# Kernel optimization log

Hardware: AMD Instinct MI355X
Metric: run time of the kernel (lower is better)

Reference implementation:

```python
import jax, jax.numpy as jnp
import numpy as np

HID = 4096
HEADS = 32
HEAD_DIM = 128
SEQ = 2048
GROUP = 128          # AWQ quantization group size along the input (K) dim
QKV_OUT = 3 * HID
ROPE_BASE = 10000.0


def dequant(qweight, scales, zeros):
    # qweight: [K, N] int; scales/zeros: [K//GROUP, N]
    s = jnp.repeat(scales, GROUP, axis=0)
    z = jnp.repeat(zeros, GROUP, axis=0)
    return (qweight.astype(jnp.float32) - z) * s


def rotate_half(x):
    x1, x2 = jnp.split(x, 2, axis=-1)
    return jnp.concatenate((-x2, x1), axis=-1)


def setup_inputs() -> dict:
    key = jax.random.key(0)
    ks = jax.random.split(key, 8)
    hidden_states = jax.random.normal(ks[0], (1, SEQ, HID), dtype=jnp.float32)
    position_ids = jnp.arange(SEQ, dtype=jnp.int32)[None, :]
    qkv_qweight = jax.random.randint(ks[1], (HID, QKV_OUT), 0, 16, dtype=jnp.int32)
    qkv_scales = jax.random.uniform(ks[2], (HID // GROUP, QKV_OUT), dtype=jnp.float32) * 0.002
    qkv_zeros = jax.random.uniform(ks[3], (HID // GROUP, QKV_OUT), dtype=jnp.float32) * 16.0
    o_qweight = jax.random.randint(ks[4], (HID, HID), 0, 16, dtype=jnp.int32)
    o_scales = jax.random.uniform(ks[5], (HID // GROUP, HID), dtype=jnp.float32) * 0.002
    o_zeros = jax.random.uniform(ks[6], (HID // GROUP, HID), dtype=jnp.float32) * 16.0
    return {"hidden_states": hidden_states, "position_ids": position_ids,
            "qkv_qweight": qkv_qweight, "qkv_scales": qkv_scales, "qkv_zeros": qkv_zeros,
            "o_qweight": o_qweight, "o_scales": o_scales, "o_zeros": o_zeros}


def reference(hidden_states, position_ids, qkv_qweight, qkv_scales, qkv_zeros,
              o_qweight, o_scales, o_zeros):
    b, s, _ = hidden_states.shape
    # --- quantized QKV projection (dequant + GEMM) ---
    w_qkv = dequant(qkv_qweight, qkv_scales, qkv_zeros)        # [HID, 3*HID]
    proj = jnp.einsum('bsk,kn->bsn', hidden_states, w_qkv)     # [b, s, 3*HID]
    xqkv = proj.reshape(b, s, 3, HEADS, HEAD_DIM)
    # [b, h, s, d]
    q = jnp.transpose(xqkv[:, :, 0], (0, 2, 1, 3))
    k = jnp.transpose(xqkv[:, :, 1], (0, 2, 1, 3))
    v = jnp.transpose(xqkv[:, :, 2], (0, 2, 1, 3))
    # --- rotary embedding (no KV cache: kv_seq_len == s) ---
    inv_freq = 1.0 / (ROPE_BASE ** (jnp.arange(0, HEAD_DIM, 2, dtype=jnp.float32) / HEAD_DIM))
    t = jnp.arange(s, dtype=jnp.float32)
    freqs = jnp.outer(t, inv_freq)                             # [s, d/2]
    emb = jnp.concatenate((freqs, freqs), axis=-1)             # [s, d]
    cos = jnp.cos(emb)[position_ids][:, None]                  # [b, 1, s, d]
    sin = jnp.sin(emb)[position_ids][:, None]
    q = q * cos + rotate_half(q) * sin
    k = k * cos + rotate_half(k) * sin
    # --- causal attention (flash_attn_func, padding_mask=None branch) ---
    scale = 1.0 / jnp.sqrt(jnp.float32(HEAD_DIM))
    scores = jnp.einsum('bhqd,bhkd->bhqk', q, k) * scale       # [b, h, s, s]
    causal = jnp.tril(jnp.ones((s, s), dtype=bool))
    scores = jnp.where(causal, scores, jnp.float32(-1e30))
    probs = jax.nn.softmax(scores, axis=-1)
    attn = jnp.einsum('bhqk,bhkd->bhqd', probs, v)             # [b, h, s, d]
    attn = jnp.transpose(attn, (0, 2, 1, 3)).reshape(b, s, HID)
    # --- quantized output projection ---
    w_o = dequant(o_qweight, o_scales, o_zeros)                # [HID, HID]
    out = jnp.einsum('bsk,kn->bsn', attn, w_o)                 # [b, s, HID]
    return out
```

## Files before the change

### kernel.cpp

```cpp
#include <hip/hip_runtime.h>
#include <hip/hip_bf16.h>

#define S_LEN 2048
#define HID_DIM 4096
#define NH 32
#define HD 128
#define NQKV 12288

typedef _Float16 half2v __attribute__((ext_vector_type(2)));
typedef _Float16 half4v __attribute__((ext_vector_type(4)));
typedef _Float16 half8v __attribute__((ext_vector_type(8)));
typedef float f32x4 __attribute__((ext_vector_type(4)));

typedef const __attribute__((address_space(1))) unsigned int* gas_u32;
typedef __attribute__((address_space(3))) unsigned int* las_u32;

__device__ inline void g2lds16(const _Float16* g, _Float16* l) {
  __builtin_amdgcn_global_load_lds((gas_u32)g, (las_u32)l, 16, 0, 0);
}

__global__ __launch_bounds__(256) void dequant_w(const int* __restrict__ W,
                                                 const float* __restrict__ scal,
                                                 const float* __restrict__ zer,
                                                 _Float16* __restrict__ Wt, int K, int N) {
  __shared__ _Float16 lT[64 * 84];
  const int k0 = blockIdx.y * 64, n0 = blockIdx.x * 64;
  const int tid = threadIdx.x, c = tid & 63, rp = tid >> 6;
  const int g = k0 >> 7;
  const float sc = scal[(size_t)g * N + n0 + c];
  const float zp = zer[(size_t)g * N + n0 + c];
#pragma unroll
  for (int i = 0; i < 8; ++i) {
    const int k = i * 8 + rp * 2;
    const float q0 = (float)W[(size_t)(k0 + k) * N + n0 + c];
    const float q1 = (float)W[(size_t)(k0 + k + 1) * N + n0 + c];
    half2v p;
    p[0] = (_Float16)((q0 - zp) * sc);
    p[1] = (_Float16)((q1 - zp) * sc);
    *(half2v*)&lT[c * 84 + k] = p;
  }
  __syncthreads();
  const int kc = tid & 7, nr0 = tid >> 3;
#pragma unroll
  for (int i = 0; i < 2; ++i) {
    const int n = nr0 + 32 * i;
    union { half8v v8; half4v v4[2]; } u;
    u.v4[0] = *(const half4v*)&lT[n * 84 + kc * 8];
    u.v4[1] = *(const half4v*)&lT[n * 84 + kc * 8 + 4];
    *(half8v*)&Wt[(size_t)(n0 + n) * K + k0 + kc * 8] = u.v8;
  }
}

__global__ __launch_bounds__(256) void conv_a(const float* __restrict__ A, _Float16* __restrict__ Af) {
  const int i = blockIdx.x * 256 + threadIdx.x;
  const float4 t = ((const float4*)A)[i];
  half4v r;
  r[0] = (_Float16)t.x; r[1] = (_Float16)t.y; r[2] = (_Float16)t.z; r[3] = (_Float16)t.w;
  ((half4v*)Af)[i] = r;
}

__device__ inline void stage128x64(const _Float16* __restrict__ gp, int K,
                                   _Float16* lp, int wave, int stR, int stC) {
  g2lds16(gp + (size_t)(wave * 16 + stR) * K + stC, lp + (wave * 2) * 512);
  g2lds16(gp + (size_t)(wave * 16 + 8 + stR) * K + stC, lp + (wave * 2 + 1) * 512);
}

template <typename CT>
__global__ __launch_bounds__(512, 2) void gemm_f16(const _Float16* __restrict__ A,
                                                   const _Float16* __restrict__ Bt,
                                                   CT* __restrict__ C, int M, int N, int K) {
  __shared__ _Float16 sA[3][2][128 * 64];
  __shared__ _Float16 sB[2][128 * 64];

  const int tid = threadIdx.x;
  const int wave = tid >> 6, lane = tid & 63;
  const int quad = lane >> 4, l16 = lane & 15;
  const int wr = wave >> 2;
  const int wc = wave & 3;
  const int NT = K >> 6;

  const _Float16* Ab = A + (size_t)(blockIdx.y * 256) * K;
  const _Float16* Bb = Bt + (size_t)(blockIdx.x * 128) * K;

  const int stR = lane >> 3;
  const int stC = ((lane & 7) ^ stR) << 3;
  const int fx = l16 & 7;

#define LDA8(buf, half, r, c) (*(const half8v*)&sA[buf][half][(r) * 64 + (((c) ^ fx) << 3)])
#define LDB8(buf, r, c) (*(const half8v*)&sB[buf][(r) * 64 + (((c) ^ fx) << 3)])

  f32x4 acc[8][2];
  const f32x4 zero4 = {0.f, 0.f, 0.f, 0.f};
#pragma unroll
  for (int am = 0; am < 8; ++am)
#pragma unroll
    for (int nb = 0; nb < 2; ++nb) acc[am][nb] = zero4;

  stage128x64(Ab, K, &sA[0][0][0], wave, stR, stC);
  stage128x64(Ab + (size_t)128 * K, K, &sA[0][1][0], wave, stR, stC);
  stage128x64(Bb, K, &sB[0][0], wave, stR, stC);
  stage128x64(Ab + 64, K, &sA[1][0][0], wave, stR, stC);
  stage128x64(Ab + (size_t)128 * K + 64, K, &sA[1][1][0], wave, stR, stC);
  stage128x64(Bb + 64, K, &sB[1][0], wave, stR, stC);
  asm volatile("s_waitcnt vmcnt(6)" ::: "memory");
  __builtin_amdgcn_s_barrier();

  int bA = 0;
  for (int t = 0; t < NT; ++t) {
    const int bB = t & 1;
    const int bA2 = (bA + 2 >= 3) ? bA - 1 : bA + 2;

    half8v af[4][2], bf[2][2];
#pragma unroll
    for (int mb = 0; mb < 4; ++mb)
#pragma unroll
      for (int ks = 0; ks < 2; ++ks)
        af[mb][ks] = LDA8(bA, wr, mb * 16 + l16, ks * 4 + quad);
#pragma unroll
    for (int nb = 0; nb < 2; ++nb)
#pragma unroll
      for (int ks = 0; ks < 2; ++ks)
        bf[nb][ks] = LDB8(bB, wc * 32 + nb * 16 + l16, ks * 4 + quad);
    if (t + 2 < NT) {
      const _Float16* Ap = Ab + (size_t)(t + 2) * 64;
      stage128x64(Ap, K, &sA[bA2][0][0], wave, stR, stC);
      stage128x64(Ap + (size_t)128 * K, K, &sA[bA2][1][0], wave, stR, stC);
    }
    __builtin_amdgcn_s_barrier();
    asm volatile("s_waitcnt lgkmcnt(0)" ::: "memory");
    __builtin_amdgcn_sched_barrier(0);
    __builtin_amdgcn_s_setprio(1);
#pragma unroll
    for (int mb = 0; mb < 4; ++mb)
#pragma unroll
      for (int nb = 0; nb < 2; ++nb)
#pragma unroll
        for (int ks = 0; ks < 2; ++ks)
          acc[mb][nb] =
              __builtin_amdgcn_mfma_f32_16x16x32_f16(af[mb][ks], bf[nb][ks], acc[mb][nb], 0, 0, 0);
    __builtin_amdgcn_s_setprio(0);
    __builtin_amdgcn_s_barrier();

#pragma unroll
    for (int mb = 0; mb < 4; ++mb)
#pragma unroll
      for (int ks = 0; ks < 2; ++ks)
        af[mb][ks] = LDA8(bA, wr, 64 + mb * 16 + l16, ks * 4 + quad);
    if (t + 2 < NT) {
      stage128x64(Bb + (size_t)(t + 2) * 64, K, &sB[bB][0], wave, stR, stC);
      asm volatile("s_waitcnt vmcnt(6)" ::: "memory");
    } else if (t + 1 < NT) {
      asm volatile("s_waitcnt vmcnt(0)" ::: "memory");
    }
    __builtin_amdgcn_s_barrier();
    asm volatile("s_waitcnt lgkmcnt(0)" ::: "memory");
    __builtin_amdgcn_sched_barrier(0);
    __builtin_amdgcn_s_setprio(1);
#pragma unroll
    for (int mb = 0; mb < 4; ++mb)
#pragma unroll
      for (int nb = 0; nb < 2; ++nb)
#pragma unroll
        for (int ks = 0; ks < 2; ++ks)
          acc[4 + mb][nb] = __builtin_amdgcn_mfma_f32_16x16x32_f16(af[mb][ks], bf[nb][ks],
                                                                   acc[4 + mb][nb], 0, 0, 0);
    __builtin_amdgcn_s_setprio(0);
    __builtin_amdgcn_s_barrier();

    bA = (bA + 1 >= 3) ? 0 : bA + 1;
  }

  const int rbase = blockIdx.y * 256 + wr * 128 + quad * 4;
  const int cbase = blockIdx.x * 128 + wc * 32 + l16;
#pragma unroll
  for (int am = 0; am < 8; ++am)
#pragma unroll
    for (int nb = 0; nb < 2; ++nb)
#pragma unroll
      for (int i = 0; i < 4; ++i)
        C[(size_t)(rbase + am * 16 + i) * N + cbase + nb * 16] = (CT)acc[am][nb][i];
#undef LDA8
#undef LDB8
}

__global__ __launch_bounds__(256) void rope_kernel(const _Float16* __restrict__ proj,
                                                   const int* __restrict__ pos,
                                                   _Float16* __restrict__ Q, _Float16* __restrict__ K,
                                                   _Float16* __restrict__ Vt) {
  const int h = blockIdx.x, sb = blockIdx.y;
  const int tid = threadIdx.x;
  const int s0 = sb * 64;

#pragma unroll
  for (int it = 0; it < 16; ++it) {
    const int idx = it * 256 + tid;
    const int sl = idx >> 6, j = idx & 63;
    const int s = s0 + sl;
    const float p = (float)pos[s];
    const float invrev = exp2f(-0.20762050593045455f * (float)j) * 0.15915494309189535f;
    const float rev = p * invrev;
    const float frac = rev - floorf(rev);
    const float sn = __builtin_amdgcn_sinf(frac);
    const float cs = __builtin_amdgcn_cosf(frac);
    const _Float16* rp = proj + (size_t)s * NQKV + h * HD;
    {
      const float x1 = (float)rp[j], x2 = (float)rp[j + 64];
      _Float16* qp = Q + ((size_t)h * S_LEN + s) * HD;
      qp[j] = (_Float16)(x1 * cs - x2 * sn);
      qp[j + 64] = (_Float16)(x2 * cs + x1 * sn);
    }
    {
      const float x1 = (float)rp[HID_DIM + j], x2 = (float)rp[HID_DIM + j + 64];
      _Float16* kp = K + ((size_t)h * S_LEN + s) * HD;
      kp[j] = (_Float16)(x1 * cs - x2 * sn);
      kp[j + 64] = (_Float16)(x2 * cs + x1 * sn);
    }
  }

  __shared__ _Float16 lV[64 * 132];
#pragma unroll
  for (int r = 0; r < 4; ++r) {
    const int cid = r * 256 + tid;
    const int sl = cid >> 4;
    const int d0 = (cid & 15) * 8;
    const _Float16* vp = proj + (size_t)(s0 + sl) * NQKV + 2 * HID_DIM + h * HD + d0;
    *(half4v*)&lV[sl * 132 + d0] = *(const half4v*)vp;
    *(half4v*)&lV[sl * 132 + d0 + 4] = *(const half4v*)(vp + 4);
  }
  __syncthreads();
#pragma unroll
  for (int it = 0; it < 32; ++it) {
    const int d = it * 4 + (tid >> 6);
    const int sl = tid & 63;
    Vt[((size_t)h * HD + d) * S_LEN + s0 + sl] = lV[sl * 132 + d];
  }
}

__global__ __launch_bounds__(256) void flash_attn(const _Float16* __restrict__ Q,
                                                  const _Float16* __restrict__ Km,
                                                  const _Float16* __restrict__ Vt,
                                                  _Float16* __restrict__ O) {
  __shared__ _Float16 lK[32 * 128];
  __shared__ _Float16 lV[128 * 32];
  __shared__ _Float16 lP[4][2][16 * 40];
  const int h = blockIdx.y;
  const int xb = blockIdx.x;
  const int qb = (xb & 1) ? (15 - (xb >> 1)) : (xb >> 1);
  const int tid = threadIdx.x;
  const int wave = tid >> 6, lane = tid & 63;
  const int quad = lane >> 4, l16 = lane & 15;
  const int q0w = qb * 128 + wave * 32;
  const float scale = 0.08838834764831845f;

  const _Float16* Qh = Q + (size_t)h * S_LEN * HD;
  const _Float16* Kh = Km + (size_t)h * S_LEN * HD;
  const _Float16* Vh = Vt + (size_t)h * HD * S_LEN;

  const int kRow0 = wave * 8 + (lane >> 4);
  const int kSlot = lane & 15;
  const int vRow0 = wave * 32 + (lane >> 2);
  const int vSlot = lane & 3;

  half8v qf[2][4];
#pragma unroll
  for (int r = 0; r < 2; ++r)
#pragma unroll
    for (int c = 0; c < 4; ++c)
      qf[r][c] = *(const half8v*)&Qh[(size_t)(q0w + r * 16 + l16) * HD + c * 32 + quad * 8];

  const f32x4 zero4 = {0.f, 0.f, 0.f, 0.f};
  f32x4 o[2][8];
  f32x4 lp[2];
#pragma unroll
  for (int r = 0; r < 2; ++r) {
    lp[r] = zero4;
#pragma unroll
    for (int c = 0; c < 8; ++c) o[r][c] = zero4;
  }

  const int ntiles = 4 * qb + 4;
  for (int kt = 0; kt < ntiles; ++kt) {
#pragma unroll
    for (int i = 0; i < 2; ++i) {
      const int row = kRow0 + i * 4;
      const int ck = kSlot ^ (row & 15);
      g2lds16(Kh + (size_t)(kt * 32 + row) * HD + ck * 8, &lK[(wave * 8 + i * 4) * 128]);
    }
#pragma unroll
    for (int i = 0; i < 2; ++i) {
      const int row = vRow0 + i * 16;
      const int cv = vSlot ^ ((row >> 1) & 3);
      g2lds16(Vh + (size_t)row * S_LEN + kt * 32 + cv * 8, &lV[(wave * 32 + i * 16) * 32]);
    }
    __syncthreads();

    half8v kf[2][4];
#pragma unroll
    for (int hf = 0; hf < 2; ++hf)
#pragma unroll
      for (int c = 0; c < 4; ++c) {
        const int slot = (c * 4 + quad) ^ l16;
        kf[hf][c] = *(const half8v*)&lK[(hf * 16 + l16) * 128 + slot * 8];
      }
    half8v vf[8];
#pragma unroll
    for (int c = 0; c < 8; ++c) {
      const int slot = quad ^ ((l16 >> 1) & 3);
      vf[c] = *(const half8v*)&lV[(c * 16 + l16) * 32 + slot * 8];
    }

    f32x4 s[2][2];
#pragma unroll
    for (int r = 0; r < 2; ++r)
#pragma unroll
      for (int hf = 0; hf < 2; ++hf) {
        s[r][hf] = zero4;
#pragma unroll
        for (int c = 0; c < 4; ++c)
          s[r][hf] = __builtin_amdgcn_mfma_f32_16x16x32_f16(qf[r][c], kf[hf][c], s[r][hf], 0, 0, 0);
      }

#pragma unroll
    for (int r = 0; r < 2; ++r) {
      float p0[4], p1[4];
#pragma unroll
      for (int i = 0; i < 4; ++i) {
        const int row = q0w + r * 16 + quad * 4 + i;
        const int col0 = kt * 32 + l16, col1 = col0 + 16;
        const float e0 = __expf(s[r][0][i] * scale);
        const float e1 = __expf(s[r][1][i] * scale);
        p0[i] = (col0 <= row) ? e0 : 0.f;
        p1[i] = (col1 <= row) ? e1 : 0.f;
        lp[r][i] += p0[i] + p1[i];
      }
      _Float16* pw = lP[wave][r];
#pragma unroll
      for (int i = 0; i < 4; ++i) {
        pw[(quad * 4 + i) * 40 + l16] = (_Float16)p0[i];
        pw[(quad * 4 + i) * 40 + l16 + 16] = (_Float16)p1[i];
      }
    }
    half8v pa[2];
#pragma unroll
    for (int r = 0; r < 2; ++r) pa[r] = *(half8v*)&lP[wave][r][l16 * 40 + quad * 8];

#pragma unroll
    for (int c = 0; c < 8; ++c)
#pragma unroll
      for (int r = 0; r < 2; ++r)
        o[r][c] = __builtin_amdgcn_mfma_f32_16x16x32_f16(pa[r], vf[c], o[r][c], 0, 0, 0);

    __syncthreads();
  }

#pragma unroll
  for (int r = 0; r < 2; ++r) {
    f32x4 ls = lp[r];
#pragma unroll
    for (int off = 1; off < 16; off <<= 1) {
#pragma unroll
      for (int i = 0; i < 4; ++i) ls[i] += __shfl_xor(ls[i], off);
    }
    f32x4 inv;
#pragma unroll
    for (int i = 0; i < 4; ++i) inv[i] = 1.f / ls[i];
#pragma unroll
    for (int c = 0; c < 8; ++c) {
#pragma unroll
      for (int i = 0; i < 4; ++i) {
        const int row = q0w + r * 16 + quad * 4 + i;
        O[(size_t)row * HID_DIM + h * HD + c * 16 + l16] = (_Float16)(o[r][c][i] * inv[i]);
      }
    }
  }
}

extern "C" void kernel_launch(void* const* d_in, const int* in_sizes, int n_in,
                              void* d_out, int out_size, void* d_ws, size_t ws_size,
                              hipStream_t stream) {
  const float* hidden = (const float*)d_in[0];
  const int* pos = (const int*)d_in[1];
  const int* qkv_w = (const int*)d_in[2];
  const float* qkv_s = (const float*)d_in[3];
  const float* qkv_z = (const float*)d_in[4];
  const int* o_w = (const int*)d_in[5];
  const float* o_s = (const float*)d_in[6];
  const float* o_z = (const float*)d_in[7];

  char* ws = (char*)d_ws;
  _Float16* Wt_qkv = (_Float16*)(ws + 0);
  _Float16* Qb = (_Float16*)(ws + 0);
  _Float16* Kb = (_Float16*)(ws + 16777216);
  _Float16* Vtb = (_Float16*)(ws + 33554432);
  _Float16* Af16 = (_Float16*)(ws + 100663296);
  _Float16* attn = (_Float16*)(ws + 100663296);
  _Float16* proj = (_Float16*)(ws + 117440512);
  _Float16* Wt_o = (_Float16*)(ws + 117440512);
  float* out = (float*)d_out;

  hipLaunchKernelGGL(dequant_w, dim3(192, 64), dim3(256), 0, stream,
                     qkv_w, qkv_s, qkv_z, Wt_qkv, 4096, 12288);
  hipLaunchKernelGGL(conv_a, dim3(8192), dim3(256), 0, stream, hidden, Af16);
  hipLaunchKernelGGL((gemm_f16<_Float16>), dim3(96, 8), dim3(512), 0, stream,
                     Af16, Wt_qkv, proj, 2048, 12288, 4096);
  hipLaunchKernelGGL(rope_kernel, dim3(32, 32), dim3(256), 0, stream, proj, pos, Qb, Kb, Vtb);
  hipLaunchKernelGGL(dequant_w, dim3(64, 64), dim3(256), 0, stream,
                     o_w, o_s, o_z, Wt_o, 4096, 4096);
  hipLaunchKernelGGL(flash_attn, dim3(16, 32), dim3(256), 0, stream, Qb, Kb, Vtb, attn);
  hipLaunchKernelGGL((gemm_f16<float>), dim3(32, 8), dim3(512), 0, stream,
                     attn, Wt_o, out, 2048, 4096, 4096);
}
```

Baseline: 770.1 us.

## Widen QKV GEMM N-tile, restructure GEMM B prefetch, pipeline flash-attn KV loads

The GEMM is templated on the N-tile width. The QKV projection now uses a 256x192 tile, giving 512 blocks in place of 768, and B is prefetched one k-step ahead in 64-row chunks with one fewer barrier per phase. Flash attention gains a 4-deep LDS ring for K/V tiles staged two iterations ahead, with vmcnt waits replacing the per-tile __syncthreads pair, so global loads overlap compute. The costs are more accumulator registers in the GEMM, more LDS in attention (which can lower occupancy), and a tail wave-quantization effect for the QKV grid.

```diff
diff --git a/kernel.cpp b/kernel.cpp
--- a/kernel.cpp
+++ b/kernel.cpp
@@ -64,13 +64,17 @@
   g2lds16(gp + (size_t)(wave * 16 + stR) * K + stC, lp + (wave * 2) * 512);
   g2lds16(gp + (size_t)(wave * 16 + 8 + stR) * K + stC, lp + (wave * 2 + 1) * 512);
 }
-
-template <typename CT>
-__global__ __launch_bounds__(512, 2) void gemm_f16(const _Float16* __restrict__ A,
+__device__ inline void stage64x64(const _Float16* __restrict__ gp, int K,
+                                  _Float16* lp, int wave, int stR, int stC) {
+  g2lds16(gp + (size_t)(wave * 8 + stR) * K + stC, lp + wave * 512);
+}
+
+template <int NBF, typename CT>
+__global__ __launch_bounds__(512, 2) void gemm_2ph(const _Float16* __restrict__ A,
                                                    const _Float16* __restrict__ Bt,
                                                    CT* __restrict__ C, int M, int N, int K) {
   __shared__ _Float16 sA[3][2][128 * 64];
-  __shared__ _Float16 sB[2][128 * 64];
+  __shared__ _Float16 sB[2][NBF * 64 * 64];
 
   const int tid = threadIdx.x;
   const int wave = tid >> 6, lane = tid & 63;
@@ -80,107 +84,110 @@
   const int NT = K >> 6;
 
   const _Float16* Ab = A + (size_t)(blockIdx.y * 256) * K;
-  const _Float16* Bb = Bt + (size_t)(blockIdx.x * 128) * K;
+  const _Float16* Bb = Bt + (size_t)(blockIdx.x * (NBF * 64)) * K;
 
   const int stR = lane >> 3;
   const int stC = ((lane & 7) ^ stR) << 3;
   const int fx = l16 & 7;
 
-#define LDA8(buf, half, r, c) (*(const half8v*)&sA[buf][half][(r) * 64 + (((c) ^ fx) << 3)])
-#define LDB8(buf, r, c) (*(const half8v*)&sB[buf][(r) * 64 + (((c) ^ fx) << 3)])
-
-  f32x4 acc[8][2];
+#define COFF(ks_) ((((ks_) * 4 + quad) ^ fx) << 3)
+#define SYNC_MFMA()                                  \
+  __builtin_amdgcn_s_barrier();                      \
+  asm volatile("s_waitcnt lgkmcnt(0)" ::: "memory"); \
+  __builtin_amdgcn_sched_barrier(0);
+
+  f32x4 acc[8][NBF];
   const f32x4 zero4 = {0.f, 0.f, 0.f, 0.f};
 #pragma unroll
-  for (int am = 0; am < 8; ++am)
-#pragma unroll
-    for (int nb = 0; nb < 2; ++nb) acc[am][nb] = zero4;
-
+  for (int m8 = 0; m8 < 8; ++m8)
+#pragma unroll
+    for (int nb = 0; nb < NBF; ++nb) acc[m8][nb] = zero4;
+
+#pragma unroll
+  for (int j = 0; j < NBF; ++j)
+    stage64x64(Bb + (size_t)(j * 64) * K, K, &sB[0][j * 4096], wave, stR, stC);
   stage128x64(Ab, K, &sA[0][0][0], wave, stR, stC);
   stage128x64(Ab + (size_t)128 * K, K, &sA[0][1][0], wave, stR, stC);
-  stage128x64(Bb, K, &sB[0][0], wave, stR, stC);
   stage128x64(Ab + 64, K, &sA[1][0][0], wave, stR, stC);
   stage128x64(Ab + (size_t)128 * K + 64, K, &sA[1][1][0], wave, stR, stC);
-  stage128x64(Bb + 64, K, &sB[1][0], wave, stR, stC);
-  asm volatile("s_waitcnt vmcnt(6)" ::: "memory");
+  asm volatile("s_waitcnt vmcnt(4)" ::: "memory");
   __builtin_amdgcn_s_barrier();
 
   int bA = 0;
   for (int t = 0; t < NT; ++t) {
     const int bB = t & 1;
     const int bA2 = (bA + 2 >= 3) ? bA - 1 : bA + 2;
-
-    half8v af[4][2], bf[2][2];
+    half8v af[4][2], bf[NBF][2];
+
 #pragma unroll
     for (int mb = 0; mb < 4; ++mb)
 #pragma unroll
       for (int ks = 0; ks < 2; ++ks)
-        af[mb][ks] = LDA8(bA, wr, mb * 16 + l16, ks * 4 + quad);
-#pragma unroll
-    for (int nb = 0; nb < 2; ++nb)
+        af[mb][ks] = *(const half8v*)&sA[bA][wr][(mb * 16 + l16) * 64 + COFF(ks)];
+#pragma unroll
+    for (int nb = 0; nb < NBF; ++nb)
 #pragma unroll
       for (int ks = 0; ks < 2; ++ks)
-        bf[nb][ks] = LDB8(bB, wc * 32 + nb * 16 + l16, ks * 4 + quad);
+        bf[nb][ks] = *(const half8v*)&sB[bB][(wc * (NBF * 16) + nb * 16 + l16) * 64 + COFF(ks)];
+    if (t + 1 < NT) {
+#pragma unroll
+      for (int j = 0; j < NBF; ++j)
+        stage64x64(Bb + (size_t)(j * 64) * K + (size_t)(t + 1) * 64, K,
+                   &sB[bB ^ 1][j * 4096], wave, stR, stC);
+    }
+    SYNC_MFMA()
+    __builtin_amdgcn_s_setprio(1);
+#pragma unroll
+    for (int mb = 0; mb < 4; ++mb)
+#pragma unroll
+      for (int nb = 0; nb < NBF; ++nb)
+#pragma unroll
+        for (int ks = 0; ks < 2; ++ks)
+          acc[mb][nb] =
+              __builtin_amdgcn_mfma_f32_16x16x32_f16(af[mb][ks], bf[nb][ks], acc[mb][nb], 0, 0, 0);
+    __builtin_amdgcn_s_setprio(0);
+
+#pragma unroll
+    for (int mb = 0; mb < 4; ++mb)
+#pragma unroll
+      for (int ks = 0; ks < 2; ++ks)
+        af[mb][ks] = *(const half8v*)&sA[bA][wr][(64 + mb * 16 + l16) * 64 + COFF(ks)];
     if (t + 2 < NT) {
       const _Float16* Ap = Ab + (size_t)(t + 2) * 64;
       stage128x64(Ap, K, &sA[bA2][0][0], wave, stR, stC);
       stage128x64(Ap + (size_t)128 * K, K, &sA[bA2][1][0], wave, stR, stC);
-    }
-    __builtin_amdgcn_s_barrier();
-    asm volatile("s_waitcnt lgkmcnt(0)" ::: "memory");
-    __builtin_amdgcn_sched_barrier(0);
-    __builtin_amdgcn_s_setprio(1);
-#pragma unroll
-    for (int mb = 0; mb < 4; ++mb)
-#pragma unroll
-      for (int nb = 0; nb < 2; ++nb)
-#pragma unroll
-        for (int ks = 0; ks < 2; ++ks)
-          acc[mb][nb] =
-              __builtin_amdgcn_mfma_f32_16x16x32_f16(af[mb][ks], bf[nb][ks], acc[mb][nb], 0, 0, 0);
-    __builtin_amdgcn_s_setprio(0);
-    __builtin_amdgcn_s_barrier();
-
-#pragma unroll
-    for (int mb = 0; mb < 4; ++mb)
-#pragma unroll
-      for (int ks = 0; ks < 2; ++ks)
-        af[mb][ks] = LDA8(bA, wr, 64 + mb * 16 + l16, ks * 4 + quad);
-    if (t + 2 < NT) {
-      stage128x64(Bb + (size_t)(t + 2) * 64, K, &sB[bB][0], wave, stR, stC);
-      asm volatile("s_waitcnt vmcnt(6)" ::: "memory");
+      asm volatile("s_waitcnt vmcnt(4)" ::: "memory");
     } else if (t + 1 < NT) {
       asm volatile("s_waitcnt vmcnt(0)" ::: "memory");
     }
-    __builtin_amdgcn_s_barrier();
-    asm volatile("s_waitcnt lgkmcnt(0)" ::: "memory");
-    __builtin_amdgcn_sched_barrier(0);
+    SYNC_MFMA()
     __builtin_amdgcn_s_setprio(1);
 #pragma unroll
     for (int mb = 0; mb < 4; ++mb)
 #pragma unroll
-      for (int nb = 0; nb < 2; ++nb)
+      for (int nb = 0; nb < NBF; ++nb)
 #pragma unroll
         for (int ks = 0; ks < 2; ++ks)
           acc[4 + mb][nb] = __builtin_amdgcn_mfma_f32_16x16x32_f16(af[mb][ks], bf[nb][ks],
                                                                    acc[4 + mb][nb], 0, 0, 0);
     __builtin_amdgcn_s_setprio(0);
-    __builtin_amdgcn_s_barrier();
 
     bA = (bA + 1 >= 3) ? 0 : bA + 1;
   }
 
   const int rbase = blockIdx.y * 256 + wr * 128 + quad * 4;
-  const int cbase = blockIdx.x * 128 + wc * 32 + l16;
-#pragma unroll
-  for (int am = 0; am < 8; ++am)
-#pragma unroll
-    for (int nb = 0; nb < 2; ++nb)
+  const int cbase = blockIdx.x * (NBF * 64) + wc * (NBF * 16) + l16;
+#pragma unroll
+  for (int m8 = 0; m8 < 8; ++m8) {
+    const int rowb = rbase + (m8 >> 2) * 64 + (m8 & 3) * 16;
+#pragma unroll
+    for (int nb = 0; nb < NBF; ++nb)
 #pragma unroll
       for (int i = 0; i < 4; ++i)
-        C[(size_t)(rbase + am * 16 + i) * N + cbase + nb * 16] = (CT)acc[am][nb][i];
-#undef LDA8
-#undef LDB8
+        C[(size_t)(rowb + i) * N + cbase + nb * 16] = (CT)acc[m8][nb][i];
+  }
+#undef COFF
+#undef SYNC_MFMA
 }
 
 __global__ __launch_bounds__(256) void rope_kernel(const _Float16* __restrict__ proj,
@@ -240,8 +247,8 @@
                                                   const _Float16* __restrict__ Km,
                                                   const _Float16* __restrict__ Vt,
                                                   _Float16* __restrict__ O) {
-  __shared__ _Float16 lK[32 * 128];
-  __shared__ _Float16 lV[128 * 32];
+  __shared__ _Float16 lK[4][32 * 128];
+  __shared__ _Float16 lV[4][128 * 32];
   __shared__ _Float16 lP[4][2][16 * 40];
   const int h = blockIdx.y;
   const int xb = blockIdx.x;
@@ -261,6 +268,21 @@
   const int vRow0 = wave * 32 + (lane >> 2);
   const int vSlot = lane & 3;
 
+  auto stage_kv = [&](int kt_, int buf_) {
+#pragma unroll
+    for (int i = 0; i < 2; ++i) {
+      const int row = kRow0 + i * 4;
+      const int ck = kSlot ^ (row & 15);
+      g2lds16(Kh + (size_t)(kt_ * 32 + row) * HD + ck * 8, &lK[buf_][(wave * 8 + i * 4) * 128]);
+    }
+#pragma unroll
+    for (int i = 0; i < 2; ++i) {
+      const int row = vRow0 + i * 16;
+      const int cv = vSlot ^ ((row >> 1) & 3);
+      g2lds16(Vh + (size_t)row * S_LEN + kt_ * 32 + cv * 8, &lV[buf_][(wave * 32 + i * 16) * 32]);
+    }
+  };
+
   half8v qf[2][4];
 #pragma unroll
   for (int r = 0; r < 2; ++r)
@@ -279,20 +301,20 @@
   }
 
   const int ntiles = 4 * qb + 4;
+  stage_kv(0, 0);
+  stage_kv(1, 1);
+
   for (int kt = 0; kt < ntiles; ++kt) {
-#pragma unroll
-    for (int i = 0; i < 2; ++i) {
-      const int row = kRow0 + i * 4;
-      const int ck = kSlot ^ (row & 15);
-      g2lds16(Kh + (size_t)(kt * 32 + row) * HD + ck * 8, &lK[(wave * 8 + i * 4) * 128]);
-    }
-#pragma unroll
-    for (int i = 0; i < 2; ++i) {
-      const int row = vRow0 + i * 16;
-      const int cv = vSlot ^ ((row >> 1) & 3);
-      g2lds16(Vh + (size_t)row * S_LEN + kt * 32 + cv * 8, &lV[(wave * 32 + i * 16) * 32]);
-    }
-    __syncthreads();
+    const int cb = kt & 3;
+    if (kt + 2 < ntiles) {
+      stage_kv(kt + 2, (kt + 2) & 3);
+      asm volatile("s_waitcnt vmcnt(8)" ::: "memory");
+    } else if (kt + 1 < ntiles) {
+      asm volatile("s_waitcnt vmcnt(4)" ::: "memory");
+    } else {
+      asm volatile("s_waitcnt vmcnt(0)" ::: "memory");
+    }
+    __builtin_amdgcn_s_barrier();
 
     half8v kf[2][4];
 #pragma unroll
@@ -300,13 +322,13 @@
 #pragma unroll
       for (int c = 0; c < 4; ++c) {
         const int slot = (c * 4 + quad) ^ l16;
-        kf[hf][c] = *(const half8v*)&lK[(hf * 16 + l16) * 128 + slot * 8];
+        kf[hf][c] = *(const half8v*)&lK[cb][(hf * 16 + l16) * 128 + slot * 8];
       }
     half8v vf[8];
 #pragma unroll
     for (int c = 0; c < 8; ++c) {
       const int slot = quad ^ ((l16 >> 1) & 3);
-      vf[c] = *(const half8v*)&lV[(c * 16 + l16) * 32 + slot * 8];
+      vf[c] = *(const half8v*)&lV[cb][(c * 16 + l16) * 32 + slot * 8];
     }
 
     f32x4 s[2][2];
@@ -349,8 +371,6 @@
 #pragma unroll
       for (int r = 0; r < 2; ++r)
         o[r][c] = __builtin_amdgcn_mfma_f32_16x16x32_f16(pa[r], vf[c], o[r][c], 0, 0, 0);
-
-    __syncthreads();
   }
 
 #pragma unroll
@@ -401,12 +421,12 @@
   hipLaunchKernelGGL(dequant_w, dim3(192, 64), dim3(256), 0, stream,
                      qkv_w, qkv_s, qkv_z, Wt_qkv, 4096, 12288);
   hipLaunchKernelGGL(conv_a, dim3(8192), dim3(256), 0, stream, hidden, Af16);
-  hipLaunchKernelGGL((gemm_f16<_Float16>), dim3(96, 8), dim3(512), 0, stream,
+  hipLaunchKernelGGL((gemm_2ph<3, _Float16>), dim3(64, 8), dim3(512), 0, stream,
                      Af16, Wt_qkv, proj, 2048, 12288, 4096);
   hipLaunchKernelGGL(rope_kernel, dim3(32, 32), dim3(256), 0, stream, proj, pos, Qb, Kb, Vtb);
   hipLaunchKernelGGL(dequant_w, dim3(64, 64), dim3(256), 0, stream,
                      o_w, o_s, o_z, Wt_o, 4096, 4096);
   hipLaunchKernelGGL(flash_attn, dim3(16, 32), dim3(256), 0, stream, Qb, Kb, Vtb, attn);
-  hipLaunchKernelGGL((gemm_f16<float>), dim3(32, 8), dim3(512), 0, stream,
+  hipLaunchKernelGGL((gemm_2ph<2, float>), dim3(32, 8), dim3(512), 0, stream,
                      attn, Wt_o, out, 2048, 4096, 4096);
 }
```

Result: faster. 719.3 us, median of 2 (-6.6%).
